# Kernel tuning notes

Measured on AMD Instinct MI355X. Metric: run time of the kernel, lower is better.

## Reference

```python
import jax, jax.numpy as jnp
import numpy as np

N_NODES = 100000


def gcn_conv(x, src, dst, W, b, n_nodes):
    # PyG GCNConv: add self-loops, sym-normalize, transform then aggregate.
    loop = jnp.arange(n_nodes, dtype=src.dtype)
    s = jnp.concatenate([src, loop])
    d = jnp.concatenate([dst, loop])
    ones = jnp.ones(s.shape[0], dtype=x.dtype)
    deg = jax.ops.segment_sum(ones, d, num_segments=n_nodes)
    dinv = jnp.where(deg > 0, jax.lax.rsqrt(deg), 0.0)
    norm = dinv[s] * dinv[d]  # [E+N]
    h = x @ W                 # [N, out]
    msg = h[s] * norm[:, None]
    out = jax.ops.segment_sum(msg, d, num_segments=n_nodes)
    return out + b


def setup_inputs() -> dict:
    key = jax.random.key(0)
    ks = jax.random.split(key, 10)
    n, f = N_NODES, 128
    x = jax.random.normal(ks[0], (n, f), dtype=jnp.float32)
    edge_index = jax.random.randint(ks[1], (2, 1600000), 0, n, dtype=jnp.int64)

    def glorot(k, fin, fout):
        lim = float(np.sqrt(6.0 / (fin + fout)))
        return jax.random.uniform(k, (fin, fout), jnp.float32, -lim, lim)

    return {
        "x": x,
        "edge_index": edge_index,
        "W1": glorot(ks[2], f, 128), "b1": jnp.zeros((128,), jnp.float32),
        "W2": glorot(ks[3], 128, 64), "b2": jnp.zeros((64,), jnp.float32),
        "W3": glorot(ks[4], 64, 32), "b3": jnp.zeros((32,), jnp.float32),
        "Wc": glorot(ks[5], 64, 1), "bc": jnp.zeros((1,), jnp.float32),
    }


def reference(x, edge_index, W1, b1, W2, b2, W3, b3, Wc, bc):
    n = x.shape[0]
    src, dst = edge_index[0], edge_index[1]
    h = jax.nn.relu(gcn_conv(x, src, dst, W1, b1, n))   # dropout: eval mode
    h = jax.nn.relu(gcn_conv(h, src, dst, W2, b2, n))
    h = jax.nn.relu(gcn_conv(h, src, dst, W3, b3, n))
    edge_feat = jnp.concatenate([h[src], h[dst]], axis=1)  # [E, 64]
    return edge_feat @ Wc + bc
```

## Files before the change

### kernel.cpp

```cpp
#include <hip/hip_runtime.h>


typedef unsigned short u16;
typedef short bfrag __attribute__((ext_vector_type(8)));
typedef float ffrag __attribute__((ext_vector_type(4)));

#define BSHIFT 8
#define MAXB   512
#define BIN_CHUNK 4096
#define BCAP   4608

static __device__ __forceinline__ float4 f4add(float4 a, float4 b) {
    return make_float4(a.x + b.x, a.y + b.y, a.z + b.z, a.w + b.w);
}

static __device__ __forceinline__ u16 f2bf(float f) {
    unsigned u = __float_as_uint(f);
    u = (u + 0x7FFFu + ((u >> 16) & 1u)) >> 16;
    return (u16)u;
}

static __device__ __forceinline__ float bflo(unsigned u) {
    return __uint_as_float(u << 16);
}
static __device__ __forceinline__ float bfhi(unsigned u) {
    return __uint_as_float(u & 0xFFFF0000u);
}
static __device__ __forceinline__ void bfacc2(float& a0, float& a1, unsigned u) {
    a0 += bflo(u);
    a1 += bfhi(u);
}
static __device__ __forceinline__ void bfacc8(float* a, uint4 u) {
    bfacc2(a[0], a[1], u.x); bfacc2(a[2], a[3], u.y);
    bfacc2(a[4], a[5], u.z); bfacc2(a[6], a[7], u.w);
}


__global__ __launch_bounds__(256) void bin_edges(const int* __restrict__ src,
                                                 const int* __restrict__ dst,
                                                 int* __restrict__ bcur,
                                                 unsigned* __restrict__ pairs,
                                                 int E, int B) {
    __shared__ int h[MAXB];
    __shared__ int base[MAXB];
    const int t = threadIdx.x;
    const int e0 = blockIdx.x * BIN_CHUNK;
    const int eEnd = min(e0 + BIN_CHUNK, E);
    for (int i = t; i < B; i += 256) h[i] = 0;
    __syncthreads();
    for (int e = e0 + t; e < eEnd; e += 256)
        atomicAdd(&h[dst[e] >> BSHIFT], 1);
    __syncthreads();
    for (int i = t; i < B; i += 256) {
        int c = h[i];
        base[i] = c ? atomicAdd(&bcur[i], c) : 0;
        h[i] = 0;
    }
    __syncthreads();
    for (int e = e0 + t; e < eEnd; e += 256) {
        int d = dst[e];
        int b = d >> BSHIFT;
        int pos = base[b] + atomicAdd(&h[b], 1);
        pairs[pos] = ((unsigned)(d & 255) << 24) | (unsigned)src[e];
    }
}

__global__ __launch_bounds__(256) void build_csr(const unsigned* __restrict__ pairs,
                                                 const int* __restrict__ bcur,
                                                 int* __restrict__ rowp,
                                                 int* __restrict__ rowe,
                                                 float* __restrict__ dinv,
                                                 int* __restrict__ ssrc, int N) {
    __shared__ int s[256];
    __shared__ int cur[256];
    const int t = threadIdx.x;
    const int b = blockIdx.x;
    const int eBeg = b * BCAP, eEnd = bcur[b];
    const int nodeBase = b << BSHIFT;
    s[t] = 0;
    __syncthreads();
    for (int e = eBeg + t; e < eEnd; e += 256)
        atomicAdd(&s[pairs[e] >> 24], 1);
    __syncthreads();
    const int v = s[t];
    #pragma unroll
    for (int off = 1; off < 256; off <<= 1) {
        int add = (t >= off) ? s[t - off] : 0;
        __syncthreads();
        s[t] += add;
        __syncthreads();
    }
    const int rp = eBeg + s[t] - v;
    const int node = nodeBase + t;
    if (node < N) {
        rowp[node] = rp;
        rowe[node] = rp + v;
        dinv[node] = rsqrtf((float)(v + 1));
    }
    cur[t] = rp;
    __syncthreads();
    for (int e = eBeg + t; e < eEnd; e += 256) {
        unsigned p = pairs[e];
        int pos = atomicAdd(&cur[p >> 24], 1);
        ssrc[pos] = (int)(p & 0xFFFFFFu);
    }
}

__global__ __launch_bounds__(256) void prep_all(const float* __restrict__ W1,
                                                u16* __restrict__ w1t,
                                                const float* __restrict__ W2,
                                                u16* __restrict__ w2t,
                                                int* __restrict__ bcur, int B) {
    int idx = blockIdx.x * 256 + threadIdx.x;
    if (idx < 128 * 128) {
        int n = idx >> 7, k = idx & 127;
        w1t[idx] = f2bf(W1[k * 128 + n]);
    } else if (idx < 128 * 128 + 64 * 128) {
        int j = idx - 128 * 128;
        int n = j >> 7, k = j & 127;
        w2t[j] = f2bf(W2[k * 64 + n]);
    }
    if (idx < B) bcur[idx] = idx * BCAP;
}

template <int FIN, int FOUT, int AMODE, bool OS, int MINW>
__global__ __launch_bounds__(256, MINW)
void gemm_mfma(const void* __restrict__ Xv, const u16* __restrict__ Wt,
               const float* __restrict__ dinv, u16* __restrict__ G, int N) {
    constexpr int NT = FOUT / 16;
    constexpr int KK = FIN / 32;
    constexpr int CB = FIN / 8;
    constexpr int ITER = (64 * CB) / 256;
    __shared__ __align__(16) u16 xs[64 * FIN];
    __shared__ float ldv[64];

    const int t = threadIdx.x;
    const int wave = t >> 6;
    const int lane = t & 63;
    const int l15 = lane & 15;
    const int quad = lane >> 4;
    const int r0 = blockIdx.x * 64;

    bfrag Bf[NT][KK];
    #pragma unroll
    for (int nt = 0; nt < NT; nt++)
        #pragma unroll
        for (int kk = 0; kk < KK; kk++)
            Bf[nt][kk] = *reinterpret_cast<const bfrag*>(
                &Wt[(size_t)(nt * 16 + l15) * FIN + kk * 32 + quad * 8]);

    if (t < 64) ldv[t] = (r0 + t < N) ? dinv[r0 + t] : 0.f;

    #pragma unroll
    for (int i = 0; i < ITER; i++) {
        int v = t + 256 * i;
        int row = v / CB;
        int cb = v - row * CB;
        uint4 pack = make_uint4(0, 0, 0, 0);
        if (r0 + row < N) {
            if (AMODE == 0) {
                const float* X = (const float*)Xv;
                const float4* p = reinterpret_cast<const float4*>(
                    &X[(size_t)(r0 + row) * FIN + cb * 8]);
                float4 lo = p[0], hi = p[1];
                pack.x = f2bf(lo.x) | ((unsigned)f2bf(lo.y) << 16);
                pack.y = f2bf(lo.z) | ((unsigned)f2bf(lo.w) << 16);
                pack.z = f2bf(hi.x) | ((unsigned)f2bf(hi.y) << 16);
                pack.w = f2bf(hi.z) | ((unsigned)f2bf(hi.w) << 16);
            } else {
                const u16* X = (const u16*)Xv;
                pack = *reinterpret_cast<const uint4*>(
                    &X[((size_t)(cb >> 1) * N + (r0 + row)) * 16 + (cb & 1) * 8]);
            }
        }
        int cbs = cb ^ (row & 7);
        *reinterpret_cast<uint4*>(&xs[row * FIN + cbs * 8]) = pack;
    }
    __syncthreads();

    ffrag acc[NT];
    #pragma unroll
    for (int nt = 0; nt < NT; nt++) {
        acc[nt][0] = 0.f; acc[nt][1] = 0.f; acc[nt][2] = 0.f; acc[nt][3] = 0.f;
    }

    const int arow = wave * 16 + l15;
    #pragma unroll
    for (int kk = 0; kk < KK; kk++) {
        int cb = (kk * 4 + quad) ^ (l15 & 7);
        bfrag a = *reinterpret_cast<const bfrag*>(&xs[arow * FIN + cb * 8]);
        #pragma unroll
        for (int nt = 0; nt < NT; nt++)
            acc[nt] = __builtin_amdgcn_mfma_f32_16x16x32_bf16(a, Bf[nt][kk], acc[nt], 0, 0, 0);
    }

    #pragma unroll
    for (int nt = 0; nt < NT; nt++)
        #pragma unroll
        for (int r = 0; r < 4; r++) {
            int rl = wave * 16 + quad * 4 + r;
            int grow = r0 + rl;
            if (grow < N) {
                u16 val = f2bf(acc[nt][r] * ldv[rl]);
                if (OS)
                    G[((size_t)nt * N + grow) * 16 + l15] = val;
                else
                    G[(size_t)grow * FOUT + nt * 16 + l15] = val;
            }
        }
}

__global__ __launch_bounds__(256) void agg1_slice(const u16* __restrict__ Gs,
                                                  const int* __restrict__ rowp,
                                                  const int* __restrict__ rowe,
                                                  const int* __restrict__ ssrc,
                                                  const float* __restrict__ dinv,
                                                  const float* __restrict__ bias,
                                                  u16* __restrict__ h1s, int N) {
    const int t = threadIdx.x;
    const unsigned slice = blockIdx.x & 7;
    const int d = (blockIdx.x >> 3) * 16 + (t >> 4);
    if (d >= N) return;
    const int lj = t & 15;
    const int eo = lj & 7;
    const int fh = lj >> 3;
    const uint4* G4 = reinterpret_cast<const uint4*>(Gs) + (size_t)slice * N * 2;

    float a[8];
    #pragma unroll
    for (int i = 0; i < 8; i++) a[i] = 0.f;
    if (eo == 0)
        bfacc8(a, G4[(size_t)d * 2 + fh]);

    int e = rowp[d];
    const int end = rowe[d];
    for (; e + 16 <= end; e += 16) {
        int sa = ssrc[e + eo];
        int sb = ssrc[e + 8 + eo];
        uint4 ua = G4[(size_t)sa * 2 + fh];
        uint4 ub = G4[(size_t)sb * 2 + fh];
        bfacc8(a, ua); bfacc8(a, ub);
    }
    for (; e + 8 <= end; e += 8) {
        int sa = ssrc[e + eo];
        bfacc8(a, G4[(size_t)sa * 2 + fh]);
    }
    if (e + eo < end) {
        int sa = ssrc[e + eo];
        bfacc8(a, G4[(size_t)sa * 2 + fh]);
    }

    #pragma unroll
    for (int m = 1; m <= 4; m <<= 1)
        #pragma unroll
        for (int i = 0; i < 8; i++)
            a[i] += __shfl_xor(a[i], m);

    if (eo == 0) {
        const float dv = dinv[d];
        const float4 b0 = reinterpret_cast<const float4*>(bias)[slice * 4 + fh * 2];
        const float4 b1 = reinterpret_cast<const float4*>(bias)[slice * 4 + fh * 2 + 1];
        float h[8];
        h[0] = fmaxf(a[0] * dv + b0.x, 0.f);
        h[1] = fmaxf(a[1] * dv + b0.y, 0.f);
        h[2] = fmaxf(a[2] * dv + b0.z, 0.f);
        h[3] = fmaxf(a[3] * dv + b0.w, 0.f);
        h[4] = fmaxf(a[4] * dv + b1.x, 0.f);
        h[5] = fmaxf(a[5] * dv + b1.y, 0.f);
        h[6] = fmaxf(a[6] * dv + b1.z, 0.f);
        h[7] = fmaxf(a[7] * dv + b1.w, 0.f);
        uint4 pk;
        pk.x = f2bf(h[0]) | ((unsigned)f2bf(h[1]) << 16);
        pk.y = f2bf(h[2]) | ((unsigned)f2bf(h[3]) << 16);
        pk.z = f2bf(h[4]) | ((unsigned)f2bf(h[5]) << 16);
        pk.w = f2bf(h[6]) | ((unsigned)f2bf(h[7]) << 16);
        reinterpret_cast<uint4*>(h1s)[((size_t)slice * N + d) * 2 + fh] = pk;
    }
}

__global__ __launch_bounds__(256) void agg2_gemm3(const u16* __restrict__ G,
                                                  const int* __restrict__ rowp,
                                                  const int* __restrict__ rowe,
                                                  const int* __restrict__ ssrc,
                                                  const float* __restrict__ dinv,
                                                  const float* __restrict__ bias,
                                                  const float* __restrict__ W3,
                                                  float* __restrict__ g3, int N) {
    __shared__ __align__(16) float wl[64 * 32];
    __shared__ __align__(16) float hl[32][68];
    const int t = threadIdx.x;
    {
        const float4* s4 = reinterpret_cast<const float4*>(W3);
        float4* d4 = reinterpret_cast<float4*>(wl);
        d4[t] = s4[t];
        d4[t + 256] = s4[t + 256];
    }
    __syncthreads();
    const int lj = t & 7;
    const int dn = t >> 3;
    const int d = blockIdx.x * 32 + dn;
    if (d >= N) return;

    const uint4* G4 = reinterpret_cast<const uint4*>(G);
    float a[8];
    #pragma unroll
    for (int i = 0; i < 8; i++) a[i] = 0.f;
    bfacc8(a, G4[(size_t)d * 8 + lj]);
    int e = rowp[d];
    const int end = rowe[d];
    for (; e + 8 <= end; e += 8) {
        int s0 = ssrc[e],     s1 = ssrc[e + 1], s2 = ssrc[e + 2], s3 = ssrc[e + 3];
        int s4 = ssrc[e + 4], s5 = ssrc[e + 5], s6 = ssrc[e + 6], s7 = ssrc[e + 7];
        uint4 u0 = G4[(size_t)s0 * 8 + lj];
        uint4 u1 = G4[(size_t)s1 * 8 + lj];
        uint4 u2 = G4[(size_t)s2 * 8 + lj];
        uint4 u3 = G4[(size_t)s3 * 8 + lj];
        uint4 u4 = G4[(size_t)s4 * 8 + lj];
        uint4 u5 = G4[(size_t)s5 * 8 + lj];
        uint4 u6 = G4[(size_t)s6 * 8 + lj];
        uint4 u7 = G4[(size_t)s7 * 8 + lj];
        bfacc8(a, u0); bfacc8(a, u1); bfacc8(a, u2); bfacc8(a, u3);
        bfacc8(a, u4); bfacc8(a, u5); bfacc8(a, u6); bfacc8(a, u7);
    }
    for (; e + 4 <= end; e += 4) {
        int s0 = ssrc[e], s1 = ssrc[e + 1], s2 = ssrc[e + 2], s3 = ssrc[e + 3];
        uint4 u0 = G4[(size_t)s0 * 8 + lj];
        uint4 u1 = G4[(size_t)s1 * 8 + lj];
        uint4 u2 = G4[(size_t)s2 * 8 + lj];
        uint4 u3 = G4[(size_t)s3 * 8 + lj];
        bfacc8(a, u0); bfacc8(a, u1); bfacc8(a, u2); bfacc8(a, u3);
    }
    for (; e < end; e++)
        bfacc8(a, G4[(size_t)ssrc[e] * 8 + lj]);
    const float dv = dinv[d];
    const float4 b0 = reinterpret_cast<const float4*>(bias)[lj * 2];
    const float4 b1 = reinterpret_cast<const float4*>(bias)[lj * 2 + 1];
    float h[8];
    h[0] = fmaxf(a[0] * dv + b0.x, 0.f);
    h[1] = fmaxf(a[1] * dv + b0.y, 0.f);
    h[2] = fmaxf(a[2] * dv + b0.z, 0.f);
    h[3] = fmaxf(a[3] * dv + b0.w, 0.f);
    h[4] = fmaxf(a[4] * dv + b1.x, 0.f);
    h[5] = fmaxf(a[5] * dv + b1.y, 0.f);
    h[6] = fmaxf(a[6] * dv + b1.z, 0.f);
    h[7] = fmaxf(a[7] * dv + b1.w, 0.f);
    *reinterpret_cast<float4*>(&hl[dn][lj * 8])     = make_float4(h[0], h[1], h[2], h[3]);
    *reinterpret_cast<float4*>(&hl[dn][lj * 8 + 4]) = make_float4(h[4], h[5], h[6], h[7]);
    float g[4] = {0.f, 0.f, 0.f, 0.f};
    #pragma unroll 4
    for (int k4 = 0; k4 < 16; k4++) {
        float4 hv = *reinterpret_cast<const float4*>(&hl[dn][k4 * 4]);
        float hs[4] = {hv.x, hv.y, hv.z, hv.w};
        #pragma unroll
        for (int p = 0; p < 4; p++) {
            float4 w = *reinterpret_cast<const float4*>(&wl[(k4 * 4 + p) * 32 + lj * 4]);
            g[0] += hs[p] * w.x; g[1] += hs[p] * w.y;
            g[2] += hs[p] * w.z; g[3] += hs[p] * w.w;
        }
    }
    *reinterpret_cast<float4*>(&g3[(size_t)d * 32 + lj * 4]) =
        make_float4(g[0] * dv, g[1] * dv, g[2] * dv, g[3] * dv);
}

__global__ __launch_bounds__(256) void aggregate_l3s(const float* __restrict__ G,
                                                     const int* __restrict__ rowp,
                                                     const int* __restrict__ rowe,
                                                     const int* __restrict__ ssrc,
                                                     const float* __restrict__ dinv,
                                                     const float* __restrict__ bias,
                                                     const float* __restrict__ Wc,
                                                     float2* __restrict__ ab, int N) {
    constexpr int L = 8;
    const int t = threadIdx.x;
    const int lj = t % L;
    const int d = blockIdx.x * 32 + t / L;
    if (d >= N) return;

    const float4* G4 = reinterpret_cast<const float4*>(G);
    float4 acc = G4[(size_t)d * L + lj];
    int e = rowp[d];
    const int end = rowe[d];
    for (; e + 8 <= end; e += 8) {
        int s0 = ssrc[e],     s1 = ssrc[e + 1], s2 = ssrc[e + 2], s3 = ssrc[e + 3];
        int s4 = ssrc[e + 4], s5 = ssrc[e + 5], s6 = ssrc[e + 6], s7 = ssrc[e + 7];
        float4 v0 = G4[(size_t)s0 * L + lj];
        float4 v1 = G4[(size_t)s1 * L + lj];
        float4 v2 = G4[(size_t)s2 * L + lj];
        float4 v3 = G4[(size_t)s3 * L + lj];
        float4 v4 = G4[(size_t)s4 * L + lj];
        float4 v5 = G4[(size_t)s5 * L + lj];
        float4 v6 = G4[(size_t)s6 * L + lj];
        float4 v7 = G4[(size_t)s7 * L + lj];
        acc = f4add(acc, f4add(f4add(f4add(v0, v1), f4add(v2, v3)),
                               f4add(f4add(v4, v5), f4add(v6, v7))));
    }
    for (; e + 4 <= end; e += 4) {
        int s0 = ssrc[e], s1 = ssrc[e + 1], s2 = ssrc[e + 2], s3 = ssrc[e + 3];
        float4 v0 = G4[(size_t)s0 * L + lj];
        float4 v1 = G4[(size_t)s1 * L + lj];
        float4 v2 = G4[(size_t)s2 * L + lj];
        float4 v3 = G4[(size_t)s3 * L + lj];
        acc = f4add(acc, f4add(f4add(v0, v1), f4add(v2, v3)));
    }
    for (; e < end; e++)
        acc = f4add(acc, G4[(size_t)ssrc[e] * L + lj]);
    const float dv = dinv[d];
    const float4 b4 = reinterpret_cast<const float4*>(bias)[lj];
    float4 h;
    h.x = fmaxf(acc.x * dv + b4.x, 0.f);
    h.y = fmaxf(acc.y * dv + b4.y, 0.f);
    h.z = fmaxf(acc.z * dv + b4.z, 0.f);
    h.w = fmaxf(acc.w * dv + b4.w, 0.f);
    const float4 wa = reinterpret_cast<const float4*>(Wc)[lj];
    const float4 wb = reinterpret_cast<const float4*>(Wc + 32)[lj];
    float p = h.x * wa.x + h.y * wa.y + h.z * wa.z + h.w * wa.w;
    float q = h.x * wb.x + h.y * wb.y + h.z * wb.z + h.w * wb.w;
    p += __shfl_xor(p, 1); q += __shfl_xor(q, 1);
    p += __shfl_xor(p, 2); q += __shfl_xor(q, 2);
    p += __shfl_xor(p, 4); q += __shfl_xor(q, 4);
    if (lj == 0) ab[d] = make_float2(p, q);
}


__global__ __launch_bounds__(256) void edge_out(const int* __restrict__ src,
                                                const int* __restrict__ dst,
                                                const float2* __restrict__ ab,
                                                const float* __restrict__ bc,
                                                float* __restrict__ out, int E) {
    int e = blockIdx.x * 256 + threadIdx.x;
    if (e < E) out[e] = ab[src[e]].x + ab[dst[e]].y + bc[0];
}

extern "C" void kernel_launch(void* const* d_in, const int* in_sizes, int n_in,
                              void* d_out, int out_size, void* d_ws, size_t ws_size,
                              hipStream_t stream) {
    const float* x  = (const float*)d_in[0];
    const int*   ei = (const int*)d_in[1];
    const float* W1 = (const float*)d_in[2];
    const float* b1 = (const float*)d_in[3];
    const float* W2 = (const float*)d_in[4];
    const float* b2 = (const float*)d_in[5];
    const float* W3 = (const float*)d_in[6];
    const float* b3 = (const float*)d_in[7];
    const float* Wc = (const float*)d_in[8];
    const float* bc = (const float*)d_in[9];
    float* out = (float*)d_out;

    const int N = in_sizes[0] / 128;
    const int E = in_sizes[1] / 2;
    const int B = (N + 255) >> BSHIFT;
    const int* src = ei;
    const int* dst = ei + E;

    size_t off = 0;
    auto alloc = [&](size_t bytes) -> void* {
        size_t o = (off + 255) & ~(size_t)255;
        off = o + bytes;
        return (void*)((char*)d_ws + o);
    };
    float* dinv = (float*)alloc((size_t)N * 4);
    int*   rowp = (int*)alloc((size_t)N * 4);
    int*   rowe = (int*)alloc((size_t)N * 4);
    int*   bcur = (int*)alloc((size_t)(B + 1) * 4);
    int*   ssrc = (int*)alloc((size_t)B * BCAP * 4);
    u16*   w1t  = (u16*)alloc(128 * 128 * 2);
    u16*   w2t  = (u16*)alloc(64 * 128 * 2);
    u16*   g16  = (u16*)alloc((size_t)N * 128 * 2);
    u16*   h1s  = (u16*)alloc((size_t)N * 128 * 2);
    u16*   g2b  = (u16*)alloc((size_t)N * 64 * 2);
    float2* ab  = (float2*)alloc((size_t)N * 8);
    (void)ws_size; (void)n_in; (void)out_size;

    unsigned* pairs = (unsigned*)g2b;
    float* g3f = (float*)g16;

    const int gE = (E + 255) / 256;
    const int gR = (N + 63) / 64;

    prep_all<<<96, 256, 0, stream>>>(W1, w1t, W2, w2t, bcur, B);
    bin_edges<<<(E + BIN_CHUNK - 1) / BIN_CHUNK, 256, 0, stream>>>(src, dst, bcur, pairs, E, B);
    build_csr<<<B, 256, 0, stream>>>(pairs, bcur, rowp, rowe, dinv, ssrc, N);

    gemm_mfma<128, 128, 0, true, 2><<<gR, 256, 0, stream>>>(x, w1t, dinv, g16, N);
    agg1_slice<<<8 * ((N + 15) / 16), 256, 0, stream>>>(g16, rowp, rowe, ssrc, dinv, b1, h1s, N);
    gemm_mfma<128, 64, 2, false, 2><<<gR, 256, 0, stream>>>(h1s, w2t, dinv, g2b, N);
    agg2_gemm3<<<(N + 31) / 32, 256, 0, stream>>>(g2b, rowp, rowe, ssrc, dinv, b2, W3, g3f, N);
    aggregate_l3s<<<(N + 31) / 32, 256, 0, stream>>>(g3f, rowp, rowe, ssrc, dinv, b3, Wc, ab, N);

    edge_out<<<gE, 256, 0, stream>>>(src, dst, ab, bc, out, E);
}
```

Measured before the change: 373.1 us.

## Assign one thread pair per node in layer-1 aggregation instead of 16 threads

The layer-1 sliced aggregation kernel used to map 16 lanes to each destination node, splitting its edges 8 ways and then combining them with shuffle reductions. It now gives each node a pair of threads, one per feature half, and each thread walks the whole edge list serially with a 4-way unrolled gather loop. This removes the shuffle reduction and the idle lanes on low-degree nodes, at the cost of less memory-level parallelism per node. It also adds load imbalance across the lanes of a wavefront, since nodes have different degrees, and each lane now gathers from a different source row, so the loads are less coalesced.

New measurement: 358.0 us. -4.0%, faster.

```diff
diff --git a/kernel.cpp b/kernel.cpp
--- a/kernel.cpp
+++ b/kernel.cpp
@@ -219,63 +219,47 @@
                                                   u16* __restrict__ h1s, int N) {
     const int t = threadIdx.x;
     const unsigned slice = blockIdx.x & 7;
-    const int d = (blockIdx.x >> 3) * 16 + (t >> 4);
+    const int fh = t & 1;
+    const int d = (blockIdx.x >> 3) * 128 + (t >> 1);
     if (d >= N) return;
-    const int lj = t & 15;
-    const int eo = lj & 7;
-    const int fh = lj >> 3;
     const uint4* G4 = reinterpret_cast<const uint4*>(Gs) + (size_t)slice * N * 2;
 
     float a[8];
     #pragma unroll
     for (int i = 0; i < 8; i++) a[i] = 0.f;
-    if (eo == 0)
-        bfacc8(a, G4[(size_t)d * 2 + fh]);
+    bfacc8(a, G4[(size_t)d * 2 + fh]);
 
     int e = rowp[d];
     const int end = rowe[d];
-    for (; e + 16 <= end; e += 16) {
-        int sa = ssrc[e + eo];
-        int sb = ssrc[e + 8 + eo];
-        uint4 ua = G4[(size_t)sa * 2 + fh];
-        uint4 ub = G4[(size_t)sb * 2 + fh];
-        bfacc8(a, ua); bfacc8(a, ub);
-    }
-    for (; e + 8 <= end; e += 8) {
-        int sa = ssrc[e + eo];
-        bfacc8(a, G4[(size_t)sa * 2 + fh]);
-    }
-    if (e + eo < end) {
-        int sa = ssrc[e + eo];
-        bfacc8(a, G4[(size_t)sa * 2 + fh]);
-    }
-
-    #pragma unroll
-    for (int m = 1; m <= 4; m <<= 1)
-        #pragma unroll
-        for (int i = 0; i < 8; i++)
-            a[i] += __shfl_xor(a[i], m);
-
-    if (eo == 0) {
-        const float dv = dinv[d];
-        const float4 b0 = reinterpret_cast<const float4*>(bias)[slice * 4 + fh * 2];
-        const float4 b1 = reinterpret_cast<const float4*>(bias)[slice * 4 + fh * 2 + 1];
-        float h[8];
-        h[0] = fmaxf(a[0] * dv + b0.x, 0.f);
-        h[1] = fmaxf(a[1] * dv + b0.y, 0.f);
-        h[2] = fmaxf(a[2] * dv + b0.z, 0.f);
-        h[3] = fmaxf(a[3] * dv + b0.w, 0.f);
-        h[4] = fmaxf(a[4] * dv + b1.x, 0.f);
-        h[5] = fmaxf(a[5] * dv + b1.y, 0.f);
-        h[6] = fmaxf(a[6] * dv + b1.z, 0.f);
-        h[7] = fmaxf(a[7] * dv + b1.w, 0.f);
-        uint4 pk;
-        pk.x = f2bf(h[0]) | ((unsigned)f2bf(h[1]) << 16);
-        pk.y = f2bf(h[2]) | ((unsigned)f2bf(h[3]) << 16);
-        pk.z = f2bf(h[4]) | ((unsigned)f2bf(h[5]) << 16);
-        pk.w = f2bf(h[6]) | ((unsigned)f2bf(h[7]) << 16);
-        reinterpret_cast<uint4*>(h1s)[((size_t)slice * N + d) * 2 + fh] = pk;
-    }
+    for (; e + 4 <= end; e += 4) {
+        int s0 = ssrc[e], s1 = ssrc[e + 1], s2 = ssrc[e + 2], s3 = ssrc[e + 3];
+        uint4 u0 = G4[(size_t)s0 * 2 + fh];
+        uint4 u1 = G4[(size_t)s1 * 2 + fh];
+        uint4 u2 = G4[(size_t)s2 * 2 + fh];
+        uint4 u3 = G4[(size_t)s3 * 2 + fh];
+        bfacc8(a, u0); bfacc8(a, u1); bfacc8(a, u2); bfacc8(a, u3);
+    }
+    for (; e < end; e++)
+        bfacc8(a, G4[(size_t)ssrc[e] * 2 + fh]);
+
+    const float dv = dinv[d];
+    const float4 b0 = reinterpret_cast<const float4*>(bias)[slice * 4 + fh * 2];
+    const float4 b1 = reinterpret_cast<const float4*>(bias)[slice * 4 + fh * 2 + 1];
+    float h[8];
+    h[0] = fmaxf(a[0] * dv + b0.x, 0.f);
+    h[1] = fmaxf(a[1] * dv + b0.y, 0.f);
+    h[2] = fmaxf(a[2] * dv + b0.z, 0.f);
+    h[3] = fmaxf(a[3] * dv + b0.w, 0.f);
+    h[4] = fmaxf(a[4] * dv + b1.x, 0.f);
+    h[5] = fmaxf(a[5] * dv + b1.y, 0.f);
+    h[6] = fmaxf(a[6] * dv + b1.z, 0.f);
+    h[7] = fmaxf(a[7] * dv + b1.w, 0.f);
+    uint4 pk;
+    pk.x = f2bf(h[0]) | ((unsigned)f2bf(h[1]) << 16);
+    pk.y = f2bf(h[2]) | ((unsigned)f2bf(h[3]) << 16);
+    pk.z = f2bf(h[4]) | ((unsigned)f2bf(h[5]) << 16);
+    pk.w = f2bf(h[6]) | ((unsigned)f2bf(h[7]) << 16);
+    reinterpret_cast<uint4*>(h1s)[((size_t)slice * N + d) * 2 + fh] = pk;
 }
 
 __global__ __launch_bounds__(256) void agg2_gemm3(const u16* __restrict__ G,
@@ -482,7 +466,7 @@
     build_csr<<<B, 256, 0, stream>>>(pairs, bcur, rowp, rowe, dinv, ssrc, N);
 
     gemm_mfma<128, 128, 0, true, 2><<<gR, 256, 0, stream>>>(x, w1t, dinv, g16, N);
-    agg1_slice<<<8 * ((N + 15) / 16), 256, 0, stream>>>(g16, rowp, rowe, ssrc, dinv, b1, h1s, N);
+    agg1_slice<<<8 * ((N + 127) / 128), 256, 0, stream>>>(g16, rowp, rowe, ssrc, dinv, b1, h1s, N);
     gemm_mfma<128, 64, 2, false, 2><<<gR, 256, 0, stream>>>(h1s, w2t, dinv, g2b, N);
     agg2_gemm3<<<(N + 31) / 32, 256, 0, stream>>>(g2b, rowp, rowe, ssrc, dinv, b2, W3, g3f, N);
     aggregate_l3s<<<(N + 31) / 32, 256, 0, stream>>>(g3f, rowp, rowe, ssrc, dinv, b3, Wc, ab, N);
```
